# Performance work log

Hardware: AMD Instinct MI355X
Metric: run time of the kernel (lower is better)

Reference implementation:

```python
import jax, jax.numpy as jnp
from jax import lax
import numpy as np

B, ENC, H, DE, T = 16384, 512, 256, 32, 64


def setup_inputs() -> dict:
    key = jax.random.key(0)
    ks = jax.random.split(key, 12)
    s = lambda fan: 1.0 / np.sqrt(fan)
    return {
        "encoded_input_series": jax.random.normal(ks[0], (B, ENC), jnp.float32),
        "final_x_val": jax.random.normal(ks[1], (B, 1), jnp.float32),
        # embed_func: Dense(DE) applied to scalar input (last dim = 1)
        "W_emb": jax.random.normal(ks[2], (1, DE), jnp.float32) * s(1),
        "b_emb": jnp.zeros((DE,), jnp.float32),
        # encode_reshape layer: Dense(H) on encoded series -> initial h
        "W_enc": jax.random.normal(ks[3], (ENC, H), jnp.float32) * s(ENC),
        "b_enc": jnp.zeros((H,), jnp.float32),
        # LSTM cell params (Keras gate order i, f, c, o)
        "W_k": jax.random.normal(ks[4], (DE, 4 * H), jnp.float32) * s(DE),
        "W_r": jax.random.normal(ks[5], (H, 4 * H), jnp.float32) * s(H),
        "b_lstm": jnp.concatenate([jnp.zeros((H,)), jnp.ones((H,)), jnp.zeros((2 * H,))]).astype(jnp.float32),
        # reduce layer: Dense(1)
        "W_red": jax.random.normal(ks[6], (H, 1), jnp.float32) * s(H),
        "b_red": jnp.zeros((1,), jnp.float32),
        "decode_length": T,
    }


def reference(encoded_input_series, final_x_val, W_emb, b_emb, W_enc, b_enc,
              W_k, W_r, b_lstm, W_red, b_red, decode_length):
    Hdim = W_r.shape[0]
    # initial hidden state from encoder summary; cell state zero-initialized
    h0 = encoded_input_series @ W_enc + b_enc            # [B, H]
    c0 = jnp.zeros_like(h0)
    # initial decoder input: embed of last observed value
    x0 = final_x_val @ W_emb + b_emb                     # [B, DE]

    def step(carry, _):
        h, c, x = carry
        gates = x @ W_k + h @ W_r + b_lstm               # [B, 4H]
        i, f, cb, o = jnp.split(gates, 4, axis=-1)
        c_new = jax.nn.sigmoid(f) * c + jax.nn.sigmoid(i) * jnp.tanh(cb)
        h_new = jax.nn.sigmoid(o) * jnp.tanh(c_new)
        y = h_new @ W_red + b_red                        # [B, 1]
        x_next = y @ W_emb + b_emb
        return (h_new, c_new, x_next), y[:, 0]

    _, ys = lax.scan(step, (h0, c0, x0), None, length=decode_length)
    return ys.T                                          # [B, T]
```

## Files before the change

### kernel.cpp

```cpp
#include <hip/hip_runtime.h>
#include <hip/hip_bf16.h>
#include <math.h>


typedef _Float16 f16x8 __attribute__((ext_vector_type(8)));
typedef float f32x4 __attribute__((ext_vector_type(4)));

#define DEV __device__ __forceinline__

constexpr int ENC = 512;
constexpr int HD  = 256;
constexpr int DE  = 32;
constexpr int TT  = 64;
constexpr int NG  = 4 * HD;
constexpr int NKT = 8;
constexpr int TS  = 528;
constexpr int BR  = 32;
constexpr int NMT = 2;

DEV bool is_f32(const void* blstm) {
  return ((const unsigned*)blstm)[256] == 0x3F800000u;
}
DEV float ldf(const void* p, size_t i, bool f32) {
  return f32 ? ((const float*)p)[i]
             : __bfloat162float(((const __hip_bfloat16*)p)[i]);
}
DEV void split2h(float v, _Float16& hi, _Float16& lo) {
  hi = (_Float16)v;
  lo = (_Float16)(v - (float)hi);
}
DEV void ld8cvt2h(const void* p, size_t i, bool f32, f16x8& hi, f16x8& lo) {
  if (f32) {
    const f32x4* q = (const f32x4*)((const float*)p + i);
    f32x4 u0 = q[0], u1 = q[1];
#pragma unroll
    for (int j = 0; j < 4; ++j) {
      float a = u0[j], b = u1[j];
      _Float16 ah = (_Float16)a, bh = (_Float16)b;
      hi[j] = ah; hi[4 + j] = bh;
      lo[j] = (_Float16)(a - (float)ah); lo[4 + j] = (_Float16)(b - (float)bh);
    }
  } else {
    const __hip_bfloat16* s = (const __hip_bfloat16*)p + i;
#pragma unroll
    for (int j = 0; j < 8; ++j) {
      float a = __bfloat162float(s[j]);
      _Float16 ah = (_Float16)a;
      hi[j] = ah;
      lo[j] = (_Float16)(a - (float)ah);
    }
  }
}
DEV f16x8 load8h(const _Float16* p) {
  return *reinterpret_cast<const f16x8*>(p);
}

constexpr float L2E = 1.44269504088896f;
DEV float sigm(float x) {
  return __builtin_amdgcn_rcpf(1.0f + __builtin_amdgcn_exp2f(-L2E * x));
}
DEV float tanh_(float x) {
  return 2.0f * __builtin_amdgcn_rcpf(1.0f + __builtin_amdgcn_exp2f(-2.0f * L2E * x)) - 1.0f;
}

__global__ __launch_bounds__(256) void pack_vec(const void* __restrict__ wemb,
                                                const void* __restrict__ bemb,
                                                const void* __restrict__ wk,
                                                const void* __restrict__ bl,
                                                const void* __restrict__ bredp,
                                                float* __restrict__ wk2,
                                                float* __restrict__ bp,
                                                float* __restrict__ bp2) {
  const bool f32 = is_f32(bl);
  int n = blockIdx.x * 256 + threadIdx.x;
  if (n >= NG) return;
  float s1 = 0.f, s2 = 0.f;
  for (int j = 0; j < DE; ++j) {
    float wkv = ldf(wk, (size_t)j * NG + n, f32);
    s1 += ldf(wemb, j, f32) * wkv;
    s2 += ldf(bemb, j, f32) * wkv;
  }
  float b = s2 + ldf(bl, n, f32);
  wk2[n] = s1;
  bp[n]  = b;
  bp2[n] = b + ldf(bredp, 0, f32) * s1;
}

__global__ __launch_bounds__(256) void pack_w(const void* __restrict__ wr,
                                              const void* __restrict__ bl,
                                              const void* __restrict__ wred,
                                              const float* __restrict__ wk2,
                                              _Float16* __restrict__ d0,
                                              _Float16* __restrict__ d1) {
  const bool f32 = is_f32(bl);
  int idx = blockIdx.x * 256 + threadIdx.x;
  if (idx >= NKT * 64 * 64) return;
  int lane = idx & 63, tile = idx >> 6;
  int nt = tile & 63, ks = tile >> 6;
  int kb = ks * 32 + ((lane >> 4) << 3);
  int n  = (nt << 4) + (lane & 15);
  float wn = wk2[n];
#pragma unroll
  for (int j = 0; j < 8; ++j) {
    int k = kb + j;
    float v = ldf(wr, (size_t)k * NG + n, f32);
    d0[idx * 8 + j] = (_Float16)v;
    d1[idx * 8 + j] = (_Float16)(v + ldf(wred, k, f32) * wn);
  }
}

__global__ __launch_bounds__(256) void pack_e(const void* __restrict__ we,
                                              const void* __restrict__ bl,
                                              _Float16* __restrict__ dhi,
                                              _Float16* __restrict__ dlo) {
  const bool f32 = is_f32(bl);
  int idx = blockIdx.x * 256 + threadIdx.x;
  if (idx >= 16 * 16 * 64) return;
  int lane = idx & 63, tile = idx >> 6;
  int nt = tile & 15, ks = tile >> 4;
  int kb = ks * 32 + ((lane >> 4) << 3);
  int n  = (nt << 4) + (lane & 15);
#pragma unroll
  for (int j = 0; j < 8; ++j) {
    float v = ldf(we, (size_t)(kb + j) * HD + n, f32);
    _Float16 h, l;
    split2h(v, h, l);
    dhi[idx * 8 + j] = h;
    dlo[idx * 8 + j] = l;
  }
}

__global__ __launch_bounds__(512)
__attribute__((amdgpu_waves_per_eu(4, 4)))
void lstm_main(
    const void* __restrict__ enc,
    const void* __restrict__ fx,
    const void* __restrict__ benc,
    const void* __restrict__ blstm,
    const void* __restrict__ wred,
    const void* __restrict__ bredp,
    const _Float16* __restrict__ pW0,
    const _Float16* __restrict__ pW1,
    const _Float16* __restrict__ pEhi,
    const _Float16* __restrict__ pElo,
    const float* __restrict__ wk2,
    const float* __restrict__ bp,
    const float* __restrict__ bp2,
    const int* __restrict__ dlen,
    void* __restrict__ out) {
  __shared__ __align__(16) _Float16 frag[2][NMT * NKT * TS];
  __shared__ __align__(16) float wredf[HD];
  __shared__ __align__(16) float bp0L[NG];
  __shared__ __align__(16) float bp2L[NG];
  __shared__ __align__(16) float wk2L[NG];
  __shared__ __align__(16) float fxL[BR];

  const bool f32 = is_f32(blstm);
  const int tid  = threadIdx.x;
  const int w    = tid >> 6;
  const int lane = tid & 63;
  const int q    = lane >> 4;
  const int cl   = lane & 15;
  const int r0   = blockIdx.x * BR;
  int Tn = dlen[0];
  if (Tn < 1 || Tn > TT) Tn = TT;

  const int aoff = lane * 8;
  const int hwb = w * TS + q * 32 + 128 * (cl >> 3) + (cl & 7);
  const int cbase = w * 32 + cl;

  const int yrow  = tid >> 4, ypart = tid & 15;
  const int ybase = ((yrow >> 4) * NKT + (ypart >> 1)) * TS +
                    ((yrow & 15) + 16 * ((ypart & 1) * 2)) * 8;

  if (tid < HD) wredf[tid] = ldf(wred, tid, f32);
  if (tid < BR) fxL[tid] = ldf(fx, r0 + tid, f32);
  bp0L[tid]        = bp[tid];
  bp0L[tid + 512]  = bp[tid + 512];
  bp2L[tid]        = bp2[tid];
  bp2L[tid + 512]  = bp2[tid + 512];
  wk2L[tid]        = wk2[tid];
  wk2L[tid + 512]  = wk2[tid + 512];
  const float bredf = ldf(bredp, 0, f32);

  f32x4 acc0[NMT][2];
  {
    float be0 = ldf(benc, w * 32 + cl, f32);
    float be1 = ldf(benc, w * 32 + 16 + cl, f32);
#pragma unroll
    for (int mt = 0; mt < NMT; ++mt) {
      acc0[mt][0] = (f32x4){be0, be0, be0, be0};
      acc0[mt][1] = (f32x4){be1, be1, be1, be1};
    }
  }
  const size_t ebase = ((size_t)(w * 2) * 64 + lane) * 8;
#pragma unroll 1
  for (int ks = 0; ks < ENC / 32; ++ks) {
    f16x8 bh[2], bl2[2];
#pragma unroll
    for (int hh = 0; hh < 2; ++hh) {
      size_t fo = ebase + (size_t)(ks * 16 + hh) * 512;
      bh[hh]  = load8h(pEhi + fo);
      bl2[hh] = load8h(pElo + fo);
    }
#pragma unroll
    for (int mt = 0; mt < NMT; ++mt) {
      f16x8 ah, al;
      ld8cvt2h(enc, (size_t)(r0 + mt * 16 + cl) * ENC + ks * 32 + q * 8, f32, ah, al);
#pragma unroll
      for (int hh = 0; hh < 2; ++hh) {
        acc0[mt][hh] = __builtin_amdgcn_mfma_f32_16x16x32_f16(ah, bh[hh],  acc0[mt][hh], 0, 0, 0);
        acc0[mt][hh] = __builtin_amdgcn_mfma_f32_16x16x32_f16(al, bh[hh],  acc0[mt][hh], 0, 0, 0);
        acc0[mt][hh] = __builtin_amdgcn_mfma_f32_16x16x32_f16(ah, bl2[hh], acc0[mt][hh], 0, 0, 0);
      }
    }
  }
#pragma unroll
  for (int mt = 0; mt < NMT; ++mt)
#pragma unroll
    for (int hh = 0; hh < 2; ++hh)
#pragma unroll
      for (int r = 0; r < 4; ++r) {
        int idx = mt * NKT * TS + hwb + r * 8 + hh * 256;
        frag[0][idx] = (_Float16)acc0[mt][hh][r];
      }

  f32x4 cst[NMT][2];
#pragma unroll
  for (int mt = 0; mt < NMT; ++mt)
#pragma unroll
    for (int hh = 0; hh < 2; ++hh) cst[mt][hh] = (f32x4){0.f, 0.f, 0.f, 0.f};

  __syncthreads();

  const _Float16* wbase0 = pW0 + ((size_t)(w * 2) * 64 + lane) * 8;
  const _Float16* wbase1 = pW1 + ((size_t)(w * 2) * 64 + lane) * 8;

  int rb = 0;
#pragma unroll 1
  for (int t = 0; t < Tn; ++t) {
    const _Float16* FH = &frag[rb][0];
    _Float16* WH = &frag[rb ^ 1][0];

    f32x4 acc[NMT][8];
    if (t == 0) {
      f32x4 fxv[NMT];
#pragma unroll
      for (int mt = 0; mt < NMT; ++mt)
        fxv[mt] = *(const f32x4*)&fxL[mt * 16 + q * 4];
#pragma unroll
      for (int nf = 0; nf < 8; ++nf) {
        int col = (nf >> 1) * 256 + (nf & 1) * 16 + cbase;
        float bb = bp0L[col], wv = wk2L[col];
#pragma unroll
        for (int mt = 0; mt < NMT; ++mt) {
          f32x4 a;
#pragma unroll
          for (int r = 0; r < 4; ++r) a[r] = bb + fxv[mt][r] * wv;
          acc[mt][nf] = a;
        }
      }
    } else {
#pragma unroll
      for (int nf = 0; nf < 8; ++nf) {
        int col = (nf >> 1) * 256 + (nf & 1) * 16 + cbase;
        float bb = bp2L[col];
#pragma unroll
        for (int mt = 0; mt < NMT; ++mt) acc[mt][nf] = (f32x4){bb, bb, bb, bb};
      }
    }

    const _Float16* wb = (t == 0) ? wbase0 : wbase1;
#pragma unroll 1
    for (int j = 0; j < 8; ++j) {
      int ks = (j + w) & 7;
#pragma unroll
      for (int half = 0; half < 2; ++half) {
        f16x8 bc[4];
#pragma unroll
        for (int p = 0; p < 4; ++p)
          bc[p] = load8h(wb +
                         (size_t)(ks * 64 + (half * 2 + (p >> 1)) * 16 + (p & 1)) * 512);
#pragma unroll
        for (int mt = 0; mt < NMT; ++mt) {
          f16x8 ah = load8h(&FH[(mt * NKT + ks) * TS + aoff]);
#pragma unroll
          for (int p = 0; p < 4; ++p)
            acc[mt][half * 4 + p] =
                __builtin_amdgcn_mfma_f32_16x16x32_f16(ah, bc[p], acc[mt][half * 4 + p], 0, 0, 0);
        }
      }
    }

    if (t > 0) {
      float sum = 0.f;
#pragma unroll
      for (int jj = 0; jj < 2; ++jj) {
        f16x8 hv = load8h(&FH[ybase + jj * 128]);
#pragma unroll
        for (int j = 0; j < 8; ++j)
          sum += (float)hv[j] * wredf[ypart * 16 + jj * 8 + j];
      }
      sum += __shfl_xor(sum, 1);
      sum += __shfl_xor(sum, 2);
      sum += __shfl_xor(sum, 4);
      sum += __shfl_xor(sum, 8);
      if (ypart == 0) {
        float y = sum + bredf;
        size_t oi = (size_t)(r0 + yrow) * TT + (t - 1);
        if (f32) ((float*)out)[oi] = y;
        else     ((__hip_bfloat16*)out)[oi] = __float2bfloat16(y);
      }
    }

#pragma unroll
    for (int mt = 0; mt < NMT; ++mt)
#pragma unroll
      for (int hh = 0; hh < 2; ++hh)
#pragma unroll
        for (int r = 0; r < 4; ++r) {
          float gi = acc[mt][0 + hh][r];
          float gf = acc[mt][2 + hh][r];
          float gc = acc[mt][4 + hh][r];
          float go = acc[mt][6 + hh][r];
          float cn = sigm(gf) * cst[mt][hh][r] + sigm(gi) * tanh_(gc);
          cst[mt][hh][r] = cn;
          float hn = sigm(go) * tanh_(cn);
          int idx = mt * NKT * TS + hwb + r * 8 + hh * 256;
          WH[idx] = (_Float16)hn;
        }
    __syncthreads();
    rb ^= 1;
  }

  {
    const _Float16* FH = &frag[rb][0];
    float sum = 0.f;
#pragma unroll
    for (int jj = 0; jj < 2; ++jj) {
      f16x8 hv = load8h(&FH[ybase + jj * 128]);
#pragma unroll
      for (int j = 0; j < 8; ++j)
        sum += (float)hv[j] * wredf[ypart * 16 + jj * 8 + j];
    }
    sum += __shfl_xor(sum, 1);
    sum += __shfl_xor(sum, 2);
    sum += __shfl_xor(sum, 4);
    sum += __shfl_xor(sum, 8);
    if (ypart == 0) {
      float y = sum + bredf;
      size_t oi = (size_t)(r0 + yrow) * TT + (Tn - 1);
      if (f32) ((float*)out)[oi] = y;
      else     ((__hip_bfloat16*)out)[oi] = __float2bfloat16(y);
    }
  }
}

extern "C" void kernel_launch(void* const* d_in, const int* in_sizes, int n_in,
                              void* d_out, int out_size, void* d_ws, size_t ws_size,
                              hipStream_t stream) {
  const void* enc  = d_in[0];
  const void* fx   = d_in[1];
  const void* wemb = d_in[2];
  const void* bemb = d_in[3];
  const void* wenc = d_in[4];
  const void* benc = d_in[5];
  const void* wk   = d_in[6];
  const void* wr   = d_in[7];
  const void* bl   = d_in[8];
  const void* wred = d_in[9];
  const void* bred = d_in[10];
  const int* dlen  = (const int*)d_in[11];

  _Float16* pW0 = (_Float16*)d_ws;
  _Float16* pW1 = pW0 + NKT * 64 * 64 * 8;
  _Float16* pEhi = pW1 + NKT * 64 * 64 * 8;
  _Float16* pElo = pEhi + 16 * 16 * 64 * 8;
  float* wk2 = (float*)(pElo + 16 * 16 * 64 * 8);
  float* bp  = wk2 + NG;
  float* bp2 = bp + NG;

  pack_vec<<<4, 256, 0, stream>>>(wemb, bemb, wk, bl, bred, wk2, bp, bp2);
  pack_w<<<128, 256, 0, stream>>>(wr, bl, wred, wk2, pW0, pW1);
  pack_e<<<64, 256, 0, stream>>>(wenc, bl, pEhi, pElo);

  int nblocks = in_sizes[1] / BR;
  lstm_main<<<nblocks, 512, 0, stream>>>(enc, fx, benc, bl, wred, bred,
                                         pW0, pW1, pEhi, pElo, wk2, bp, bp2,
                                         dlen, d_out);
}
```

Baseline: 941.8 us.

## Prescale gate weights by log2e and merge LSTM gate reciprocals

```diff
diff --git a/kernel.cpp b/kernel.cpp
--- a/kernel.cpp
+++ b/kernel.cpp
@@ -18,12 +18,17 @@
 constexpr int BR  = 32;
 constexpr int NMT = 2;
 
+constexpr float L2E = 1.44269504088896f;
+
 DEV bool is_f32(const void* blstm) {
   return ((const unsigned*)blstm)[256] == 0x3F800000u;
 }
 DEV float ldf(const void* p, size_t i, bool f32) {
   return f32 ? ((const float*)p)[i]
              : __bfloat162float(((const __hip_bfloat16*)p)[i]);
+}
+DEV float gscale(int n) {
+  return ((n >> 8) == 2) ? (2.0f * L2E) : L2E;
 }
 DEV void split2h(float v, _Float16& hi, _Float16& lo) {
   hi = (_Float16)v;
@@ -55,22 +60,15 @@
   return *reinterpret_cast<const f16x8*>(p);
 }
 
-constexpr float L2E = 1.44269504088896f;
-DEV float sigm(float x) {
-  return __builtin_amdgcn_rcpf(1.0f + __builtin_amdgcn_exp2f(-L2E * x));
-}
-DEV float tanh_(float x) {
-  return 2.0f * __builtin_amdgcn_rcpf(1.0f + __builtin_amdgcn_exp2f(-2.0f * L2E * x)) - 1.0f;
-}
-
 __global__ __launch_bounds__(256) void pack_vec(const void* __restrict__ wemb,
                                                 const void* __restrict__ bemb,
                                                 const void* __restrict__ wk,
                                                 const void* __restrict__ bl,
                                                 const void* __restrict__ bredp,
-                                                float* __restrict__ wk2,
-                                                float* __restrict__ bp,
-                                                float* __restrict__ bp2) {
+                                                float* __restrict__ wk2n,
+                                                float* __restrict__ wk2s,
+                                                float* __restrict__ bps,
+                                                float* __restrict__ bp2s) {
   const bool f32 = is_f32(bl);
   int n = blockIdx.x * 256 + threadIdx.x;
   if (n >= NG) return;
@@ -81,15 +79,17 @@
     s2 += ldf(bemb, j, f32) * wkv;
   }
   float b = s2 + ldf(bl, n, f32);
-  wk2[n] = s1;
-  bp[n]  = b;
-  bp2[n] = b + ldf(bredp, 0, f32) * s1;
+  float sc = gscale(n);
+  wk2n[n] = s1;
+  wk2s[n] = s1 * sc;
+  bps[n]  = b * sc;
+  bp2s[n] = (b + ldf(bredp, 0, f32) * s1) * sc;
 }
 
 __global__ __launch_bounds__(256) void pack_w(const void* __restrict__ wr,
                                               const void* __restrict__ bl,
                                               const void* __restrict__ wred,
-                                              const float* __restrict__ wk2,
+                                              const float* __restrict__ wk2n,
                                               _Float16* __restrict__ d0,
                                               _Float16* __restrict__ d1) {
   const bool f32 = is_f32(bl);
@@ -99,13 +99,14 @@
   int nt = tile & 63, ks = tile >> 6;
   int kb = ks * 32 + ((lane >> 4) << 3);
   int n  = (nt << 4) + (lane & 15);
-  float wn = wk2[n];
+  float wn = wk2n[n];
+  float sc = gscale(n);
 #pragma unroll
   for (int j = 0; j < 8; ++j) {
     int k = kb + j;
     float v = ldf(wr, (size_t)k * NG + n, f32);
-    d0[idx * 8 + j] = (_Float16)v;
-    d1[idx * 8 + j] = (_Float16)(v + ldf(wred, k, f32) * wn);
+    d0[idx * 8 + j] = (_Float16)(v * sc);
+    d1[idx * 8 + j] = (_Float16)((v + ldf(wred, k, f32) * wn) * sc);
   }
 }
 
@@ -143,9 +144,9 @@
     const _Float16* __restrict__ pW1,
     const _Float16* __restrict__ pEhi,
     const _Float16* __restrict__ pElo,
-    const float* __restrict__ wk2,
-    const float* __restrict__ bp,
-    const float* __restrict__ bp2,
+    const float* __restrict__ wk2s,
+    const float* __restrict__ bps,
+    const float* __restrict__ bp2s,
     const int* __restrict__ dlen,
     void* __restrict__ out) {
   __shared__ __align__(16) _Float16 frag[2][NMT * NKT * TS];
@@ -175,12 +176,12 @@
 
   if (tid < HD) wredf[tid] = ldf(wred, tid, f32);
   if (tid < BR) fxL[tid] = ldf(fx, r0 + tid, f32);
-  bp0L[tid]        = bp[tid];
-  bp0L[tid + 512]  = bp[tid + 512];
-  bp2L[tid]        = bp2[tid];
-  bp2L[tid + 512]  = bp2[tid + 512];
-  wk2L[tid]        = wk2[tid];
-  wk2L[tid + 512]  = wk2[tid + 512];
+  bp0L[tid]        = bps[tid];
+  bp0L[tid + 512]  = bps[tid + 512];
+  bp2L[tid]        = bp2s[tid];
+  bp2L[tid + 512]  = bp2s[tid + 512];
+  wk2L[tid]        = wk2s[tid];
+  wk2L[tid + 512]  = wk2s[tid + 512];
   const float bredf = ldf(bredp, 0, f32);
 
   f32x4 acc0[NMT][2];
@@ -323,9 +324,17 @@
           float gf = acc[mt][2 + hh][r];
           float gc = acc[mt][4 + hh][r];
           float go = acc[mt][6 + hh][r];
-          float cn = sigm(gf) * cst[mt][hh][r] + sigm(gi) * tanh_(gc);
+          float P = __builtin_amdgcn_exp2f(-gi);
+          float F = __builtin_amdgcn_exp2f(-gf);
+          float Q = __builtin_amdgcn_exp2f(-gc);
+          float S = __builtin_amdgcn_exp2f(-go);
+          float p1 = 1.0f + P, q1 = 1.0f + Q, f1 = 1.0f + F, s1 = 1.0f + S;
+          float pq = p1 * q1;
+          float num = cst[mt][hh][r] * pq + (1.0f - Q) * f1;
+          float cn  = num * __builtin_amdgcn_rcpf(f1 * pq);
           cst[mt][hh][r] = cn;
-          float hn = sigm(go) * tanh_(cn);
+          float R = __builtin_amdgcn_exp2f(-2.0f * L2E * cn);
+          float hn = (1.0f - R) * __builtin_amdgcn_rcpf(s1 * (1.0f + R));
           int idx = mt * NKT * TS + hwb + r * 8 + hh * 256;
           WH[idx] = (_Float16)hn;
         }
@@ -376,16 +385,17 @@
   _Float16* pW1 = pW0 + NKT * 64 * 64 * 8;
   _Float16* pEhi = pW1 + NKT * 64 * 64 * 8;
   _Float16* pElo = pEhi + 16 * 16 * 64 * 8;
-  float* wk2 = (float*)(pElo + 16 * 16 * 64 * 8);
-  float* bp  = wk2 + NG;
-  float* bp2 = bp + NG;
-
-  pack_vec<<<4, 256, 0, stream>>>(wemb, bemb, wk, bl, bred, wk2, bp, bp2);
-  pack_w<<<128, 256, 0, stream>>>(wr, bl, wred, wk2, pW0, pW1);
+  float* wk2n = (float*)(pElo + 16 * 16 * 64 * 8);
+  float* wk2s = wk2n + NG;
+  float* bps  = wk2s + NG;
+  float* bp2s = bps + NG;
+
+  pack_vec<<<4, 256, 0, stream>>>(wemb, bemb, wk, bl, bred, wk2n, wk2s, bps, bp2s);
+  pack_w<<<128, 256, 0, stream>>>(wr, bl, wred, wk2n, pW0, pW1);
   pack_e<<<64, 256, 0, stream>>>(wenc, bl, pEhi, pElo);
 
   int nblocks = in_sizes[1] / BR;
   lstm_main<<<nblocks, 512, 0, stream>>>(enc, fx, benc, bl, wred, bred,
-                                         pW0, pW1, pEhi, pElo, wk2, bp, bp2,
+                                         pW0, pW1, pEhi, pElo, wk2s, bps, bp2s,
                                          dlen, d_out);
 }
```

Result: faster. 860.4 us (-8.6%).
